# Kernel tuning notes

Hardware: AMD Instinct MI355X
Metric: run time of the kernel (lower is better)

## Reference

```python
import jax, jax.numpy as jnp
import numpy as np

B, IN, H = 16384, 128, 512
NH = 4
HD = H // NH


def setup_inputs() -> dict:
    key = jax.random.key(0)
    ks = jax.random.split(key, 20)
    s = lambda k, shape: jax.random.normal(k, shape, dtype=jnp.float32) * 0.05
    return {
        "x": jax.random.normal(ks[0], (B, IN), dtype=jnp.float32),
        "hidden_left": jax.random.normal(ks[1], (B, H), dtype=jnp.float32),
        "hidden_up": jax.random.normal(ks[2], (B, H), dtype=jnp.float32),
        "hidden_prev": jax.random.normal(ks[3], (B, H), dtype=jnp.float32),
        # input_proj
        "W_in": s(ks[4], (H, IN)),
        "b_in": jnp.zeros((H,), jnp.float32),
        # MultiheadAttention (packed qkv in-proj + out-proj), torch convention W:[out,in]
        "attn_in_w": s(ks[5], (3 * H, H)),
        "attn_in_b": jnp.zeros((3 * H,), jnp.float32),
        "attn_out_w": s(ks[6], (H, H)),
        "attn_out_b": jnp.zeros((H,), jnp.float32),
        # spatial_gate: Linear(3H -> H) then sigmoid
        "W_gate": s(ks[7], (H, 3 * H)),
        "b_gate": jnp.zeros((H,), jnp.float32),
        # GRUCell (torch layout: [3H, .] with r,z,n blocks)
        "gru_w_ih": s(ks[8], (3 * H, IN)),
        "gru_w_hh": s(ks[9], (3 * H, H)),
        "gru_b_ih": jnp.zeros((3 * H,), jnp.float32),
        "gru_b_hh": jnp.zeros((3 * H,), jnp.float32),
    }


def reference(x, hidden_left, hidden_up, hidden_prev,
              W_in, b_in, attn_in_w, attn_in_b, attn_out_w, attn_out_b,
              W_gate, b_gate, gru_w_ih, gru_w_hh, gru_b_ih, gru_b_hh):
    # input projection
    x_proj = x @ W_in.T + b_in  # [B, H]

    # spatial attention over the 2 neighbor states
    sp = jnp.stack([hidden_left, hidden_up], axis=1)          # [B, 2, H]
    qkv = sp @ attn_in_w.T + attn_in_b                        # [B, 2, 3H]
    q, k, v = jnp.split(qkv, 3, axis=-1)
    q = q.reshape(-1, 2, NH, HD)
    k = k.reshape(-1, 2, NH, HD)
    v = v.reshape(-1, 2, NH, HD)
    scores = jnp.einsum("bqhd,bkhd->bhqk", q, k) / jnp.sqrt(jnp.float32(HD))
    attn = jax.nn.softmax(scores, axis=-1)                    # [B, NH, 2, 2]
    ctx = jnp.einsum("bhqk,bkhd->bqhd", attn, v).reshape(-1, 2, H)
    sp_out = ctx @ attn_out_w.T + attn_out_b                  # [B, 2, H]
    spatial_combined = sp_out.mean(axis=1)                    # [B, H]

    # gated blend into previous hidden
    gate_in = jnp.concatenate([hidden_prev, spatial_combined, x_proj], axis=1)
    gate = jax.nn.sigmoid(gate_in @ W_gate.T + b_gate)
    enhanced_prev = hidden_prev + gate * spatial_combined

    # GRUCell(x, enhanced_prev), torch gate order r, z, n
    gi = x @ gru_w_ih.T + gru_b_ih                            # [B, 3H]
    gh = enhanced_prev @ gru_w_hh.T + gru_b_hh                # [B, 3H]
    i_r, i_z, i_n = jnp.split(gi, 3, axis=1)
    h_r, h_z, h_n = jnp.split(gh, 3, axis=1)
    r = jax.nn.sigmoid(i_r + h_r)
    z = jax.nn.sigmoid(i_z + h_z)
    n = jnp.tanh(i_n + r * h_n)
    new_hidden = (1.0 - z) * n + z * enhanced_prev
    # dropout is identity in eval mode
    return new_hidden
```

## Files before the change

### kernel.cpp

```cpp
#include <hip/hip_runtime.h>
#include <hip/hip_bf16.h>
#include <stdint.h>


#define NB 16384
#define NHEADS 4

typedef __attribute__((ext_vector_type(8))) __bf16 bf16x8;
typedef __attribute__((ext_vector_type(4))) float f32x4;
typedef __attribute__((ext_vector_type(8))) unsigned short u16x8;

__device__ __forceinline__ unsigned short f2bf(float f) {
  union { float f; unsigned int u; } v; v.f = f;
  unsigned int u = v.u;
  unsigned int r = (u + 0x7fffu + ((u >> 16) & 1u)) >> 16;
  return (unsigned short)r;
}
__device__ __forceinline__ float bf2f(unsigned short h) {
  union { unsigned int u; float f; } v; v.u = ((unsigned int)h) << 16;
  return v.f;
}
__device__ __forceinline__ float sigmoidf_(float x) {
  return 1.0f / (1.0f + __expf(-x));
}

#define J0 (512 * 128 / 8)
#define J1 (1536 * 128 / 8)
#define J2 (1536 * 512 / 8)
#define J3 (512 * 512 / 8)
#define J4 (512 * 1536 / 8)
#define J5 (1536 * 512 / 8)
#define J6 (NB * 128 / 8)
#define J7 (NB * 512 / 8)
#define J8 (NB * 512 / 8)
#define C1 (J0)
#define C2 (C1 + J1)
#define C3 (C2 + J2)
#define C4 (C3 + J3)
#define C5 (C4 + J4)
#define C6 (C5 + J5)
#define C7 (C6 + J6)
#define C8 (C7 + J7)
#define CT (C8 + J8)

struct CvtJobs {
  const float* src[9];
  unsigned short* dst[9];
};

__global__ void cvt_multi(CvtJobs j) {
  int g = blockIdx.x * blockDim.x + threadIdx.x;
  if (g >= CT) return;
  int k, base;
  if (g < C4) {
    if (g < C2) {
      if (g < C1) { k = 0; base = 0; } else { k = 1; base = C1; }
    } else {
      if (g < C3) { k = 2; base = C2; } else { k = 3; base = C3; }
    }
  } else {
    if (g < C6) {
      if (g < C5) { k = 4; base = C4; } else { k = 5; base = C5; }
    } else {
      if (g < C7) { k = 6; base = C6; }
      else if (g < C8) { k = 7; base = C7; }
      else { k = 8; base = C8; }
    }
  }
  int local = g - base;
  const float4* s = (const float4*)j.src[k] + (size_t)local * 2;
  float4 a = s[0], b = s[1];
  u16x8 o;
  o[0] = f2bf(a.x); o[1] = f2bf(a.y); o[2] = f2bf(a.z); o[3] = f2bf(a.w);
  o[4] = f2bf(b.x); o[5] = f2bf(b.y); o[6] = f2bf(b.z); o[7] = f2bf(b.w);
  *((u16x8*)j.dst[k] + local) = o;
}

__global__ void pack_hp(const float* __restrict__ hp,
                        unsigned short* __restrict__ gate_in) {
  int t = blockIdx.x * blockDim.x + threadIdx.x;
  int b = t >> 6;
  int j = (t & 63) * 8;
  const float4* s = (const float4*)(hp + (size_t)b * 512 + j);
  float4 a = s[0], c = s[1];
  u16x8 o;
  o[0] = f2bf(a.x); o[1] = f2bf(a.y); o[2] = f2bf(a.z); o[3] = f2bf(a.w);
  o[4] = f2bf(c.x); o[5] = f2bf(c.y); o[6] = f2bf(c.z); o[7] = f2bf(c.w);
  *(u16x8*)(gate_in + (size_t)b * 1536 + j) = o;
}

__device__ __forceinline__ void gl_lds16(const unsigned short* g, unsigned short* l) {
  __builtin_amdgcn_global_load_lds(
      (const __attribute__((address_space(1))) void*)g,
      (__attribute__((address_space(3))) void*)l, 16, 0, 0);
}

template <int EPI>
__global__ __launch_bounds__(512, 1) void gemm_big(
    const unsigned short* __restrict__ A, int lda,
    const unsigned short* __restrict__ W, int ldw,
    const float* __restrict__ bias, const float* __restrict__ bias2,
    int K, int ntx,
    unsigned short* __restrict__ outb, int ldob,
    unsigned short* __restrict__ outb2, int ldob2) {
  __shared__ unsigned short lds[65536];
  unsigned short* Asb = lds;
  unsigned short* Bsb = lds + 32768;
  const int tid = threadIdx.x;
  const int lane = tid & 63;
  const int wave = tid >> 6;

  const int nwg = gridDim.x;
  const int cpx = nwg >> 3;
  const int bid = blockIdx.x;
  const int id = (bid & 7) * cpx + (bid >> 3);
  const int bx = id % ntx;
  const int by = id / ntx;

  const int m0 = by * 256;
  const int n0 = bx * 256;
  const int ar0 = (wave >> 2) * 64;
  const int br0 = (wave & 3) * 32;

  f32x4 acc[4][4][2] = {};

  const int srow = tid >> 3;
  const int presw = (tid & 7) ^ (srow & 7);
  const unsigned short* Ag = A + (size_t)(m0 + srow) * lda + presw * 8;
  const unsigned short* Wg = W + (size_t)(n0 + srow) * ldw + presw * 8;
  unsigned short* Asd = Asb + tid * 8;
  unsigned short* Wsd = Bsb + tid * 8;

  auto stageA = [&](int buf, int h, int k0) {
    const unsigned short* s = Ag + (size_t)(h * 128) * lda + k0;
    unsigned short* d = Asd + buf * 16384 + h * 8192;
    gl_lds16(s, d);
    gl_lds16(s + (size_t)64 * lda, d + 4096);
  };
  auto stageB = [&](int buf, int h, int k0) {
    const unsigned short* s = Wg + (size_t)(h * 128) * ldw + k0;
    unsigned short* d = Wsd + buf * 16384 + h * 8192;
    gl_lds16(s, d);
    gl_lds16(s + (size_t)64 * ldw, d + 4096);
  };

  const int lrow = lane & 15;
  const int kq = (lane >> 4) * 8;
  const int sw = (lrow & 7) << 3;
  const int NT = K >> 6;

  stageA(0, 0, 0);
  stageB(0, 0, 0);
  stageB(0, 1, 0);
  stageA(0, 1, 0);
  asm volatile("s_waitcnt vmcnt(4)" ::: "memory");
  __builtin_amdgcn_s_barrier();

  bf16x8 a[4][2], b0[2][2], b1[2][2];

#define RD_A(X, H)                                                            \
  _Pragma("unroll") for (int m = 0; m < 4; ++m)                               \
  _Pragma("unroll") for (int kk = 0; kk < 2; ++kk)                            \
      a[m][kk] = *(const bf16x8*)&Asb[(X) * 16384 +                           \
                                      ((H) * 128 + ar0 + m * 16 + lrow) * 64 +\
                                      ((kk * 32 + kq) ^ sw)];
#define RD_B(X, H, DST)                                                       \
  _Pragma("unroll") for (int n = 0; n < 2; ++n)                               \
  _Pragma("unroll") for (int kk = 0; kk < 2; ++kk)                            \
      DST[n][kk] = *(const bf16x8*)&Bsb[(X) * 16384 +                         \
                                        ((H) * 128 + br0 + n * 16 + lrow) * 64 + \
                                        ((kk * 32 + kq) ^ sw)];
#define MFMA_Q(Q, BF)                                                         \
  __builtin_amdgcn_s_setprio(1);                                              \
  _Pragma("unroll") for (int m = 0; m < 4; ++m)                               \
  _Pragma("unroll") for (int n = 0; n < 2; ++n)                               \
  _Pragma("unroll") for (int kk = 0; kk < 2; ++kk)                            \
      acc[Q][m][n] = __builtin_amdgcn_mfma_f32_16x16x32_bf16(                 \
          a[m][kk], BF[n][kk], acc[Q][m][n], 0, 0, 0);                        \
  __builtin_amdgcn_s_setprio(0);
#define LGKM0                                                                 \
  asm volatile("s_waitcnt lgkmcnt(0)" ::: "memory");                          \
  __builtin_amdgcn_sched_barrier(0);
#define BAR __builtin_amdgcn_s_barrier();

  for (int t = 0; t < NT - 1; ++t) {
    const int X = t & 1, Y = X ^ 1;
    const int kn = (t + 1) << 6;
    RD_A(X, 0)
    RD_B(X, 0, b0)
    stageA(Y, 0, kn);
    stageB(Y, 0, kn);
    asm volatile("s_waitcnt vmcnt(4)" ::: "memory");
    BAR LGKM0
    MFMA_Q(0, b0)
    BAR
    RD_B(X, 1, b1)
    stageB(Y, 1, kn);
    BAR LGKM0
    MFMA_Q(1, b1)
    BAR
    RD_A(X, 1)
    stageA(Y, 1, kn);
    BAR LGKM0
    MFMA_Q(2, b1)
    BAR
    asm volatile("s_waitcnt vmcnt(4)" ::: "memory");
    BAR
    __builtin_amdgcn_sched_barrier(0);
    MFMA_Q(3, b0)
    BAR
  }
  {
    const int X = (NT - 1) & 1;
    RD_A(X, 0)
    RD_B(X, 0, b0)
    asm volatile("s_waitcnt vmcnt(0)" ::: "memory");
    BAR LGKM0
    MFMA_Q(0, b0)
    RD_B(X, 1, b1)
    LGKM0
    MFMA_Q(1, b1)
    RD_A(X, 1)
    LGKM0
    MFMA_Q(2, b1)
    MFMA_Q(3, b0)
  }
#undef RD_A
#undef RD_B
#undef MFMA_Q
#undef LGKM0
#undef BAR

  __syncthreads();
  unsigned short* ob = outb;
  int ld = ldob, ncof = n0;
  const float* bp = bias;
  if constexpr (EPI == 2) {
    if (n0 >= 512) { ob = outb2; ld = ldob2; ncof = n0 - 512; bp = bias2; }
  }
  const int qr[4] = {0, 0, 128, 128};
  const int qc[4] = {0, 128, 128, 0};
  const int ri = (lane >> 4) << 2;
#pragma unroll
  for (int q = 0; q < 4; ++q) {
#pragma unroll
    for (int n = 0; n < 2; ++n) {
      const int col = qc[q] + br0 + n * 16 + lrow;
      const float bv = bp ? bp[ncof + col] : 0.0f;
      const int g8 = col >> 3, c7 = col & 7;
#pragma unroll
      for (int m = 0; m < 4; ++m)
#pragma unroll
        for (int i = 0; i < 4; ++i) {
          const int row = qr[q] + ar0 + m * 16 + ri + i;
          lds[row * 256 + ((g8 ^ (row & 7)) << 3) + c7] =
              f2bf(acc[q][m][n][i] + bv);
        }
    }
  }
  __syncthreads();
#pragma unroll
  for (int jj = 0; jj < 16; ++jj) {
    int c = jj * 512 + tid;
    int row = c >> 5;
    int slot = c & 31;
    u16x8 v = *(const u16x8*)&lds[row * 256 + ((slot ^ (row & 7)) << 3)];
    *(u16x8*)&ob[(size_t)(m0 + row) * ld + ncof + slot * 8] = v;
  }
}

__global__ __launch_bounds__(512, 1) void g7_gru(
    const unsigned short* __restrict__ A, int lda,
    const unsigned short* __restrict__ W, int ldw,
    const float* __restrict__ b_hh, int K, int ntx,
    const unsigned short* __restrict__ gi,
    const unsigned short* __restrict__ enh,
    float* __restrict__ out) {
  __shared__ unsigned short lds[65536];
  unsigned short* Asb = lds;
  unsigned short* Bsb = lds + 16384;
  const int tid = threadIdx.x;
  const int lane = tid & 63;
  const int wave = tid >> 6;

  const int nwg = gridDim.x;
  const int cpx = nwg >> 3;
  const int bid = blockIdx.x;
  const int id = (bid & 7) * cpx + (bid >> 3);
  const int bx = id % ntx;
  const int by = id / ntx;

  const int m0 = by * 128;
  const int j0 = bx * 128;
  const int wm = (wave >> 2) * 64;
  const int wj = (wave & 3) * 32;

  f32x4 acc[4][6] = {};

  const int srow = tid >> 3;
  const int presw = (tid & 7) ^ (srow & 7);
  const unsigned short* Ag = A + (size_t)(m0 + srow) * lda + presw * 8;
  unsigned short* Asd = Asb + tid * 8;
  unsigned short* Bsd = Bsb + tid * 8;

  auto stage = [&](int buf, int k0) {
    gl_lds16(Ag + k0, Asd + buf * 8192);
    gl_lds16(Ag + (size_t)64 * lda + k0, Asd + buf * 8192 + 4096);
#pragma unroll
    for (int l = 0; l < 6; ++l) {
      const int gate = l >> 1;
      const int rr = (l & 1) * 64 + srow;
      gl_lds16(W + (size_t)(gate * 512 + j0 + rr) * ldw + presw * 8 + k0,
               Bsd + buf * 24576 + l * 4096);
    }
  };

  stage(0, 0);
  int cur = 0;
  const int lrow = lane & 15;
  const int kq = (lane >> 4) * 8;
  const int sw = (lrow & 7) << 3;

  for (int k0 = 0; k0 < K; k0 += 64) {
    if (k0 + 64 < K) {
      stage(cur ^ 1, k0 + 64);
      asm volatile("s_waitcnt vmcnt(8)" ::: "memory");
    } else {
      asm volatile("s_waitcnt vmcnt(0)" ::: "memory");
    }
    __builtin_amdgcn_s_barrier();
    const unsigned short* Ab = Asb + cur * 8192;
    const unsigned short* Bb = Bsb + cur * 24576;
    bf16x8 a[4][2], b[6][2];
#pragma unroll
    for (int m = 0; m < 4; ++m)
#pragma unroll
      for (int kk = 0; kk < 2; ++kk)
        a[m][kk] = *(const bf16x8*)&Ab[(wm + m * 16 + lrow) * 64 +
                                       ((kk * 32 + kq) ^ sw)];
#pragma unroll
    for (int f = 0; f < 6; ++f)
#pragma unroll
      for (int kk = 0; kk < 2; ++kk) {
        const int brow = (f >> 1) * 128 + wj + (f & 1) * 16 + lrow;
        b[f][kk] = *(const bf16x8*)&Bb[brow * 64 + ((kk * 32 + kq) ^ sw)];
      }
    __builtin_amdgcn_s_setprio(1);
#pragma unroll
    for (int m = 0; m < 4; ++m)
#pragma unroll
      for (int f = 0; f < 6; ++f)
#pragma unroll
        for (int kk = 0; kk < 2; ++kk)
          acc[m][f] = __builtin_amdgcn_mfma_f32_16x16x32_bf16(a[m][kk], b[f][kk],
                                                              acc[m][f], 0, 0, 0);
    __builtin_amdgcn_s_setprio(0);
    __builtin_amdgcn_s_barrier();
    cur ^= 1;
  }

  const int r0 = m0 + wm + ((lane >> 4) << 2);
#pragma unroll
  for (int jj = 0; jj < 2; ++jj) {
    const int j = j0 + wj + jj * 16 + lrow;
    const float bhr = b_hh[j];
    const float bhz = b_hh[512 + j];
    const float bhn = b_hh[1024 + j];
#pragma unroll
    for (int m = 0; m < 4; ++m) {
#pragma unroll
      for (int i = 0; i < 4; ++i) {
        const int row = r0 + m * 16 + i;
        const size_t gb = (size_t)row * 1536 + j;
        float ir = bf2f(gi[gb]);
        float iz = bf2f(gi[gb + 512]);
        float in_ = bf2f(gi[gb + 1024]);
        float hr = acc[m][jj][i] + bhr;
        float hz = acc[m][2 + jj][i] + bhz;
        float hn = acc[m][4 + jj][i] + bhn;
        float rr = sigmoidf_(ir + hr);
        float zz = sigmoidf_(iz + hz);
        float nn = tanhf(in_ + rr * hn);
        float ev = bf2f(enh[(size_t)row * 512 + j]);
        out[(size_t)row * 512 + j] = (1.0f - zz) * nn + zz * ev;
      }
    }
  }
}

template <int EPI>
__global__ __launch_bounds__(256, 2) void gemm_bt(
    const unsigned short* __restrict__ A, int lda,
    const unsigned short* __restrict__ W, int ldw,
    const float* __restrict__ bias, int K, int ntx,
    unsigned short* __restrict__ outb, int ldob,
    const unsigned short* __restrict__ gin) {
  __shared__ unsigned short As[2][128 * 64];
  __shared__ unsigned short Ws[2][128 * 64];
  const int tid = threadIdx.x;
  const int lane = tid & 63;
  const int wave = tid >> 6;

  const int nwg = gridDim.x;
  const int cpx = nwg >> 3;
  const int bid = blockIdx.x;
  const int id = (bid & 7) * cpx + (bid >> 3);
  const int bx = id % ntx;
  const int by = id / ntx;

  const int m0 = by * 128;
  const int n0 = bx * 128;
  const int wm = (wave >> 1) * 64;
  const int wn = (wave & 1) * 64;

  f32x4 acc[4][4] = {};

  const int srow = tid >> 3;
  const int sslot = (tid & 7) ^ (srow & 7);
  const unsigned short* Ag = A + (size_t)(m0 + srow) * lda + sslot * 8;
  const unsigned short* Wg = W + (size_t)(n0 + srow) * ldw + sslot * 8;
  unsigned short* Asd = &As[0][tid * 8];
  unsigned short* Wsd = &Ws[0][tid * 8];

  auto stage = [&](int buf, int k0) {
#pragma unroll
    for (int i = 0; i < 4; ++i) {
      gl_lds16(Ag + (size_t)(i * 32) * lda + k0, Asd + buf * 8192 + i * 2048);
      gl_lds16(Wg + (size_t)(i * 32) * ldw + k0, Wsd + buf * 8192 + i * 2048);
    }
  };

  stage(0, 0);
  int cur = 0;
  const int lrow = lane & 15;
  const int kq = (lane >> 4) * 8;
  const int sw = (lrow & 7) << 3;

  for (int k0 = 0; k0 < K; k0 += 64) {
    if (k0 + 64 < K) {
      stage(cur ^ 1, k0 + 64);
      asm volatile("s_waitcnt vmcnt(8)" ::: "memory");
    } else {
      asm volatile("s_waitcnt vmcnt(0)" ::: "memory");
    }
    __builtin_amdgcn_s_barrier();
#pragma unroll
    for (int kk = 0; kk < 2; ++kk) {
      const int kr = kk * 32 + kq;
      const int ki = kr ^ sw;
      bf16x8 af[4], wf[4];
#pragma unroll
      for (int m = 0; m < 4; ++m)
        af[m] = *(const bf16x8*)&As[cur][(wm + m * 16 + lrow) * 64 + ki];
#pragma unroll
      for (int n = 0; n < 4; ++n)
        wf[n] = *(const bf16x8*)&Ws[cur][(wn + n * 16 + lrow) * 64 + ki];
#pragma unroll
      for (int m = 0; m < 4; ++m)
#pragma unroll
        for (int n = 0; n < 4; ++n)
          acc[m][n] = __builtin_amdgcn_mfma_f32_16x16x32_bf16(af[m], wf[n],
                                                              acc[m][n], 0, 0, 0);
    }
    __builtin_amdgcn_s_barrier();
    cur ^= 1;
  }

  if constexpr (EPI == 1) {
    const int r0 = m0 + wm + ((lane >> 4) << 2);
    const int c0 = n0 + wn + lrow;
#pragma unroll
    for (int n = 0; n < 4; ++n) {
      const int col = c0 + n * 16;
      const float bv = bias ? bias[col] : 0.0f;
#pragma unroll
      for (int m = 0; m < 4; ++m) {
#pragma unroll
        for (int i = 0; i < 4; ++i) {
          const int row = r0 + m * 16 + i;
          float g = sigmoidf_(acc[m][n][i] + bv);
          float hpv = bf2f(gin[(size_t)row * 1536 + col]);
          float sc = bf2f(gin[(size_t)row * 1536 + 512 + col]);
          float e = hpv + g * sc;
          outb[(size_t)row * 512 + col] = f2bf(e);
        }
      }
    }
  } else {
    unsigned short* Cs = &As[0][0];
    const int r0l = wm + ((lane >> 4) << 2);
    const int c0l = wn + lrow;
#pragma unroll
    for (int n = 0; n < 4; ++n) {
      const int col = c0l + n * 16;
      const float bv = bias ? bias[n0 + col] : 0.0f;
#pragma unroll
      for (int m = 0; m < 4; ++m)
#pragma unroll
        for (int i = 0; i < 4; ++i)
          Cs[(r0l + m * 16 + i) * 128 + col] = f2bf(acc[m][n][i] + bv);
    }
    __syncthreads();
#pragma unroll
    for (int jj = 0; jj < 8; ++jj) {
      int c = jj * 256 + tid;
      int row = c >> 4;
      int slot = c & 15;
      u16x8 v = *(const u16x8*)&Cs[row * 128 + slot * 8];
      *(u16x8*)&outb[(size_t)(m0 + row) * ldob + n0 + slot * 8] = v;
    }
  }
}

__global__ void attn_fuse(const unsigned short* __restrict__ qkvl,
                          const unsigned short* __restrict__ qkvu,
                          unsigned short* __restrict__ ctx) {
  int t = blockIdx.x * blockDim.x + threadIdx.x;
  int g = t >> 4;
  int l = t & 15;
  int b = g >> 2, h = g & 3;
  const size_t base = (size_t)b * 1536 + h * 128 + l * 8;
  u16x8 q0 = *(const u16x8*)(qkvl + base);
  u16x8 k0 = *(const u16x8*)(qkvl + base + 512);
  u16x8 v0 = *(const u16x8*)(qkvl + base + 1024);
  u16x8 q1 = *(const u16x8*)(qkvu + base);
  u16x8 k1 = *(const u16x8*)(qkvu + base + 512);
  u16x8 v1 = *(const u16x8*)(qkvu + base + 1024);
  float s00 = 0.f, s01 = 0.f, s10 = 0.f, s11 = 0.f;
  float v0f[8], v1f[8];
#pragma unroll
  for (int i = 0; i < 8; ++i) {
    float q0f = bf2f(q0[i]), q1f = bf2f(q1[i]);
    float k0f = bf2f(k0[i]), k1f = bf2f(k1[i]);
    v0f[i] = bf2f(v0[i]); v1f[i] = bf2f(v1[i]);
    s00 += q0f * k0f; s01 += q0f * k1f;
    s10 += q1f * k0f; s11 += q1f * k1f;
  }
#pragma unroll
  for (int off = 1; off < 16; off <<= 1) {
    s00 += __shfl_xor(s00, off);
    s01 += __shfl_xor(s01, off);
    s10 += __shfl_xor(s10, off);
    s11 += __shfl_xor(s11, off);
  }
  const float scale = 0.0883883476483184f;
  s00 *= scale; s01 *= scale; s10 *= scale; s11 *= scale;
  float m0 = fmaxf(s00, s01), m1 = fmaxf(s10, s11);
  float a00 = __expf(s00 - m0), a01 = __expf(s01 - m0);
  float a10 = __expf(s10 - m1), a11 = __expf(s11 - m1);
  float c0 = 0.5f * (a00 / (a00 + a01) + a10 / (a10 + a11));
  float c1 = 0.5f * (a01 / (a00 + a01) + a11 / (a10 + a11));
  u16x8 o;
#pragma unroll
  for (int i = 0; i < 8; ++i) o[i] = f2bf(c0 * v0f[i] + c1 * v1f[i]);
  *(u16x8*)(ctx + (size_t)b * 512 + h * 128 + l * 8) = o;
}

extern "C" void kernel_launch(void* const* d_in, const int* in_sizes, int n_in,
                              void* d_out, int out_size, void* d_ws, size_t ws_size,
                              hipStream_t stream) {
  const float* x = (const float*)d_in[0];
  const float* hl = (const float*)d_in[1];
  const float* hu = (const float*)d_in[2];
  const float* hp = (const float*)d_in[3];
  const float* W_in = (const float*)d_in[4];
  const float* b_in = (const float*)d_in[5];
  const float* attn_in_w = (const float*)d_in[6];
  const float* attn_in_b = (const float*)d_in[7];
  const float* attn_out_w = (const float*)d_in[8];
  const float* attn_out_b = (const float*)d_in[9];
  const float* W_gate = (const float*)d_in[10];
  const float* b_gate = (const float*)d_in[11];
  const float* gru_w_ih = (const float*)d_in[12];
  const float* gru_w_hh = (const float*)d_in[13];
  const float* gru_b_ih = (const float*)d_in[14];
  const float* gru_b_hh = (const float*)d_in[15];

  char* ws = (char*)d_ws;
  size_t off = 0;
  auto alloc = [&](size_t bytes) {
    void* p = ws + off;
    off += (bytes + 255) & ~(size_t)255;
    return p;
  };
  unsigned short* wComb = (unsigned short*)alloc((size_t)2048 * 128 * 2);
  unsigned short* wAin  = (unsigned short*)alloc((size_t)1536 * 512 * 2);
  unsigned short* wAout = (unsigned short*)alloc((size_t)512 * 512 * 2);
  unsigned short* wGate = (unsigned short*)alloc((size_t)512 * 1536 * 2);
  unsigned short* wHh   = (unsigned short*)alloc((size_t)1536 * 512 * 2);
  unsigned short* xb   = (unsigned short*)alloc((size_t)NB * 128 * 2);
  unsigned short* hlub = (unsigned short*)alloc((size_t)2 * NB * 512 * 2);
  unsigned short* gate_in = (unsigned short*)alloc((size_t)NB * 1536 * 2);
  unsigned short* qkvb = (unsigned short*)alloc((size_t)2 * NB * 1536 * 2);
  unsigned short* ctxb = (unsigned short*)alloc((size_t)NB * 512 * 2);
  unsigned short* enhb = (unsigned short*)alloc((size_t)NB * 512 * 2);
  unsigned short* qkvl = qkvb;
  unsigned short* qkvu = qkvb + (size_t)NB * 1536;
  unsigned short* gi = qkvl;

  (void)ws_size; (void)in_sizes; (void)n_in; (void)out_size;

  const int T = 256;

  CvtJobs jobs;
  jobs.src[0] = W_in;       jobs.dst[0] = wComb;
  jobs.src[1] = gru_w_ih;   jobs.dst[1] = wComb + (size_t)512 * 128;
  jobs.src[2] = attn_in_w;  jobs.dst[2] = wAin;
  jobs.src[3] = attn_out_w; jobs.dst[3] = wAout;
  jobs.src[4] = W_gate;     jobs.dst[4] = wGate;
  jobs.src[5] = gru_w_hh;   jobs.dst[5] = wHh;
  jobs.src[6] = x;          jobs.dst[6] = xb;
  jobs.src[7] = hl;         jobs.dst[7] = hlub;
  jobs.src[8] = hu;         jobs.dst[8] = hlub + (size_t)NB * 512;
  cvt_multi<<<(CT + T - 1) / T, T, 0, stream>>>(jobs);
  pack_hp<<<NB * 64 / T, T, 0, stream>>>(hp, gate_in);

  const int MTB = NB / 256;
  const int MTS = NB / 128;

  gemm_big<0><<<6 * 2 * MTB, dim3(512), 0, stream>>>(hlub, 512, wAin, 512,
                                                     attn_in_b, nullptr, 512, 6,
                                                     qkvb, 1536, nullptr, 0);
  attn_fuse<<<NB * NHEADS * 16 / T, T, 0, stream>>>(qkvl, qkvu, ctxb);
  gemm_bt<0><<<4 * MTS, T, 0, stream>>>(ctxb, 512, wAout, 512, attn_out_b,
                                        512, 4,
                                        gate_in + 512, 1536, nullptr);
  gemm_big<2><<<8 * MTB, dim3(512), 0, stream>>>(xb, 128, wComb, 128,
                                                 b_in, gru_b_ih, 128, 8,
                                                 gate_in + 1024, 1536, gi, 1536);
  gemm_bt<1><<<4 * MTS, T, 0, stream>>>(gate_in, 1536, wGate, 1536, b_gate,
                                        1536, 4,
                                        enhb, 512, gate_in);
  g7_gru<<<4 * MTS, dim3(512), 0, stream>>>(enhb, 512, wHh, 512, gru_b_hh,
                                            512, 4, gi, enhb, (float*)d_out);
}
```

Baseline: 271.1 us.

## Fuse QKV projection with 2-token attention and interleave neighbor rows

Hidden_left and hidden_up rows are interleaved during bf16 conversion so each 128-row tile holds both neighbors of 64 batch elements. A new kernel computes the per-head Q/K/V projection tile and the attention softmax/mix in LDS, writing only the context. This removes the round trip of the full QKV intermediate through global memory and one launch. The hidden_prev pack is folded into the conversion kernel. The cost is a smaller per-block N tile (384 columns) with more LDS traffic and epilogue work inside the GEMM.

```diff
diff --git a/kernel.cpp b/kernel.cpp
--- a/kernel.cpp
+++ b/kernel.cpp
@@ -4,7 +4,6 @@
 
 
 #define NB 16384
-#define NHEADS 4
 
 typedef __attribute__((ext_vector_type(8))) __bf16 bf16x8;
 typedef __attribute__((ext_vector_type(4))) float f32x4;
@@ -33,6 +32,7 @@
 #define J6 (NB * 128 / 8)
 #define J7 (NB * 512 / 8)
 #define J8 (NB * 512 / 8)
+#define J9 (NB * 512 / 8)
 #define C1 (J0)
 #define C2 (C1 + J1)
 #define C3 (C2 + J2)
@@ -41,11 +41,12 @@
 #define C6 (C5 + J5)
 #define C7 (C6 + J6)
 #define C8 (C7 + J7)
-#define CT (C8 + J8)
+#define C9 (C8 + J8)
+#define CT (C9 + J9)
 
 struct CvtJobs {
-  const float* src[9];
-  unsigned short* dst[9];
+  const float* src[10];
+  unsigned short* dst[10];
 };
 
 __global__ void cvt_multi(CvtJobs j) {
@@ -64,7 +65,8 @@
     } else {
       if (g < C7) { k = 6; base = C6; }
       else if (g < C8) { k = 7; base = C7; }
-      else { k = 8; base = C8; }
+      else if (g < C9) { k = 8; base = C8; }
+      else { k = 9; base = C9; }
     }
   }
   int local = g - base;
@@ -73,20 +75,12 @@
   u16x8 o;
   o[0] = f2bf(a.x); o[1] = f2bf(a.y); o[2] = f2bf(a.z); o[3] = f2bf(a.w);
   o[4] = f2bf(b.x); o[5] = f2bf(b.y); o[6] = f2bf(b.z); o[7] = f2bf(b.w);
-  *((u16x8*)j.dst[k] + local) = o;
-}
-
-__global__ void pack_hp(const float* __restrict__ hp,
-                        unsigned short* __restrict__ gate_in) {
-  int t = blockIdx.x * blockDim.x + threadIdx.x;
-  int b = t >> 6;
-  int j = (t & 63) * 8;
-  const float4* s = (const float4*)(hp + (size_t)b * 512 + j);
-  float4 a = s[0], c = s[1];
-  u16x8 o;
-  o[0] = f2bf(a.x); o[1] = f2bf(a.y); o[2] = f2bf(a.z); o[3] = f2bf(a.w);
-  o[4] = f2bf(c.x); o[5] = f2bf(c.y); o[6] = f2bf(c.z); o[7] = f2bf(c.w);
-  *(u16x8*)(gate_in + (size_t)b * 1536 + j) = o;
+  size_t didx;
+  if (k == 7)      didx = ((size_t)(local >> 6) << 7) + (local & 63);
+  else if (k == 8) didx = ((size_t)(local >> 6) << 7) + 64 + (local & 63);
+  else if (k == 9) didx = (size_t)(local >> 6) * 192 + (local & 63);
+  else             didx = (size_t)local;
+  *((u16x8*)j.dst[k] + didx) = o;
 }
 
 __device__ __forceinline__ void gl_lds16(const unsigned short* g, unsigned short* l) {
@@ -269,6 +263,155 @@
   }
 }
 
+__global__ __launch_bounds__(512, 1) void qkva(
+    const unsigned short* __restrict__ A,
+    const unsigned short* __restrict__ W,
+    const float* __restrict__ bias,
+    unsigned short* __restrict__ ctx) {
+  __shared__ unsigned short lds[65536];
+  unsigned short* Asb = lds;
+  unsigned short* Bsb = lds + 16384;
+  const int tid = threadIdx.x;
+  const int lane = tid & 63;
+  const int wave = tid >> 6;
+
+  const int nwg = gridDim.x;
+  const int cpx = nwg >> 3;
+  const int bid = blockIdx.x;
+  const int id = (bid & 7) * cpx + (bid >> 3);
+  const int bx = id & 3;
+  const int by = id >> 2;
+
+  const int m0 = by * 128;
+  const int h0 = bx * 128;
+  const int wm = (wave >> 2) * 64;
+  const int wj = (wave & 3) * 32;
+
+  f32x4 acc[4][6] = {};
+
+  const int srow = tid >> 3;
+  const int presw = (tid & 7) ^ (srow & 7);
+  const unsigned short* Ag = A + (size_t)(m0 + srow) * 512 + presw * 8;
+  unsigned short* Asd = Asb + tid * 8;
+  unsigned short* Bsd = Bsb + tid * 8;
+
+  auto stage = [&](int buf, int k0) {
+    gl_lds16(Ag + k0, Asd + buf * 8192);
+    gl_lds16(Ag + (size_t)64 * 512 + k0, Asd + buf * 8192 + 4096);
+#pragma unroll
+    for (int l = 0; l < 6; ++l) {
+      const int gate = l >> 1;
+      const int rr = (l & 1) * 64 + srow;
+      gl_lds16(W + (size_t)(gate * 512 + h0 + rr) * 512 + presw * 8 + k0,
+               Bsd + buf * 24576 + l * 4096);
+    }
+  };
+
+  stage(0, 0);
+  int cur = 0;
+  const int lrow = lane & 15;
+  const int kq = (lane >> 4) * 8;
+  const int sw = (lrow & 7) << 3;
+
+  for (int k0 = 0; k0 < 512; k0 += 64) {
+    if (k0 + 64 < 512) {
+      stage(cur ^ 1, k0 + 64);
+      asm volatile("s_waitcnt vmcnt(8)" ::: "memory");
+    } else {
+      asm volatile("s_waitcnt vmcnt(0)" ::: "memory");
+    }
+    __builtin_amdgcn_s_barrier();
+    const unsigned short* Ab = Asb + cur * 8192;
+    const unsigned short* Bb = Bsb + cur * 24576;
+    bf16x8 a[4][2], b[6][2];
+#pragma unroll
+    for (int m = 0; m < 4; ++m)
+#pragma unroll
+      for (int kk = 0; kk < 2; ++kk)
+        a[m][kk] = *(const bf16x8*)&Ab[(wm + m * 16 + lrow) * 64 +
+                                       ((kk * 32 + kq) ^ sw)];
+#pragma unroll
+    for (int f = 0; f < 6; ++f)
+#pragma unroll
+      for (int kk = 0; kk < 2; ++kk) {
+        const int brow = (f >> 1) * 128 + wj + (f & 1) * 16 + lrow;
+        b[f][kk] = *(const bf16x8*)&Bb[brow * 64 + ((kk * 32 + kq) ^ sw)];
+      }
+    __builtin_amdgcn_s_setprio(1);
+#pragma unroll
+    for (int m = 0; m < 4; ++m)
+#pragma unroll
+      for (int f = 0; f < 6; ++f)
+#pragma unroll
+        for (int kk = 0; kk < 2; ++kk)
+          acc[m][f] = __builtin_amdgcn_mfma_f32_16x16x32_bf16(a[m][kk], b[f][kk],
+                                                              acc[m][f], 0, 0, 0);
+    __builtin_amdgcn_s_setprio(0);
+    __builtin_amdgcn_s_barrier();
+    cur ^= 1;
+  }
+
+  __syncthreads();
+  const int ri = (lane >> 4) << 2;
+#pragma unroll
+  for (int f = 0; f < 6; ++f) {
+    const int gate = f >> 1;
+    const int col = wj + (f & 1) * 16 + lrow;
+    const float bv = bias[gate * 512 + h0 + col];
+#pragma unroll
+    for (int m = 0; m < 4; ++m)
+#pragma unroll
+      for (int i = 0; i < 4; ++i) {
+        const int row = wm + m * 16 + ri + i;
+        lds[gate * 17408 + row * 136 + col] = f2bf(acc[m][f][i] + bv);
+      }
+  }
+  __syncthreads();
+
+  const int l = tid & 15;
+  const int grp = tid >> 4;
+#pragma unroll
+  for (int it = 0; it < 2; ++it) {
+    const int p = it * 32 + grp;
+    const int r0 = 2 * p, r1 = 2 * p + 1;
+    u16x8 q0 = *(const u16x8*)&lds[r0 * 136 + l * 8];
+    u16x8 q1 = *(const u16x8*)&lds[r1 * 136 + l * 8];
+    u16x8 k0 = *(const u16x8*)&lds[17408 + r0 * 136 + l * 8];
+    u16x8 k1 = *(const u16x8*)&lds[17408 + r1 * 136 + l * 8];
+    u16x8 v0 = *(const u16x8*)&lds[34816 + r0 * 136 + l * 8];
+    u16x8 v1 = *(const u16x8*)&lds[34816 + r1 * 136 + l * 8];
+    float s00 = 0.f, s01 = 0.f, s10 = 0.f, s11 = 0.f;
+    float v0f[8], v1f[8];
+#pragma unroll
+    for (int i = 0; i < 8; ++i) {
+      float q0f = bf2f(q0[i]), q1f = bf2f(q1[i]);
+      float k0f = bf2f(k0[i]), k1f = bf2f(k1[i]);
+      v0f[i] = bf2f(v0[i]); v1f[i] = bf2f(v1[i]);
+      s00 += q0f * k0f; s01 += q0f * k1f;
+      s10 += q1f * k0f; s11 += q1f * k1f;
+    }
+#pragma unroll
+    for (int off = 1; off < 16; off <<= 1) {
+      s00 += __shfl_xor(s00, off);
+      s01 += __shfl_xor(s01, off);
+      s10 += __shfl_xor(s10, off);
+      s11 += __shfl_xor(s11, off);
+    }
+    const float scale = 0.0883883476483184f;
+    s00 *= scale; s01 *= scale; s10 *= scale; s11 *= scale;
+    float mx0 = fmaxf(s00, s01), mx1 = fmaxf(s10, s11);
+    float a00 = __expf(s00 - mx0), a01 = __expf(s01 - mx0);
+    float a10 = __expf(s10 - mx1), a11 = __expf(s11 - mx1);
+    float c0 = 0.5f * (a00 / (a00 + a01) + a10 / (a10 + a11));
+    float c1 = 0.5f * (a01 / (a00 + a01) + a11 / (a10 + a11));
+    u16x8 o;
+#pragma unroll
+    for (int i = 0; i < 8; ++i) o[i] = f2bf(c0 * v0f[i] + c1 * v1f[i]);
+    const int bglob = (m0 >> 1) + p;
+    *(u16x8*)&ctx[(size_t)bglob * 512 + h0 + l * 8] = o;
+  }
+}
+
 __global__ __launch_bounds__(512, 1) void g7_gru(
     const unsigned short* __restrict__ A, int lda,
     const unsigned short* __restrict__ W, int ldw,
@@ -510,50 +653,6 @@
       *(u16x8*)&outb[(size_t)(m0 + row) * ldob + n0 + slot * 8] = v;
     }
   }
-}
-
-__global__ void attn_fuse(const unsigned short* __restrict__ qkvl,
-                          const unsigned short* __restrict__ qkvu,
-                          unsigned short* __restrict__ ctx) {
-  int t = blockIdx.x * blockDim.x + threadIdx.x;
-  int g = t >> 4;
-  int l = t & 15;
-  int b = g >> 2, h = g & 3;
-  const size_t base = (size_t)b * 1536 + h * 128 + l * 8;
-  u16x8 q0 = *(const u16x8*)(qkvl + base);
-  u16x8 k0 = *(const u16x8*)(qkvl + base + 512);
-  u16x8 v0 = *(const u16x8*)(qkvl + base + 1024);
-  u16x8 q1 = *(const u16x8*)(qkvu + base);
-  u16x8 k1 = *(const u16x8*)(qkvu + base + 512);
-  u16x8 v1 = *(const u16x8*)(qkvu + base + 1024);
-  float s00 = 0.f, s01 = 0.f, s10 = 0.f, s11 = 0.f;
-  float v0f[8], v1f[8];
-#pragma unroll
-  for (int i = 0; i < 8; ++i) {
-    float q0f = bf2f(q0[i]), q1f = bf2f(q1[i]);
-    float k0f = bf2f(k0[i]), k1f = bf2f(k1[i]);
-    v0f[i] = bf2f(v0[i]); v1f[i] = bf2f(v1[i]);
-    s00 += q0f * k0f; s01 += q0f * k1f;
-    s10 += q1f * k0f; s11 += q1f * k1f;
-  }
-#pragma unroll
-  for (int off = 1; off < 16; off <<= 1) {
-    s00 += __shfl_xor(s00, off);
-    s01 += __shfl_xor(s01, off);
-    s10 += __shfl_xor(s10, off);
-    s11 += __shfl_xor(s11, off);
-  }
-  const float scale = 0.0883883476483184f;
-  s00 *= scale; s01 *= scale; s10 *= scale; s11 *= scale;
-  float m0 = fmaxf(s00, s01), m1 = fmaxf(s10, s11);
-  float a00 = __expf(s00 - m0), a01 = __expf(s01 - m0);
-  float a10 = __expf(s10 - m1), a11 = __expf(s11 - m1);
-  float c0 = 0.5f * (a00 / (a00 + a01) + a10 / (a10 + a11));
-  float c1 = 0.5f * (a01 / (a00 + a01) + a11 / (a10 + a11));
-  u16x8 o;
-#pragma unroll
-  for (int i = 0; i < 8; ++i) o[i] = f2bf(c0 * v0f[i] + c1 * v1f[i]);
-  *(u16x8*)(ctx + (size_t)b * 512 + h * 128 + l * 8) = o;
 }
 
 extern "C" void kernel_launch(void* const* d_in, const int* in_sizes, int n_in,
@@ -589,14 +688,12 @@
   unsigned short* wGate = (unsigned short*)alloc((size_t)512 * 1536 * 2);
   unsigned short* wHh   = (unsigned short*)alloc((size_t)1536 * 512 * 2);
   unsigned short* xb   = (unsigned short*)alloc((size_t)NB * 128 * 2);
-  unsigned short* hlub = (unsigned short*)alloc((size_t)2 * NB * 512 * 2);
+  unsigned short* hlib = (unsigned short*)alloc((size_t)2 * NB * 512 * 2);
   unsigned short* gate_in = (unsigned short*)alloc((size_t)NB * 1536 * 2);
   unsigned short* qkvb = (unsigned short*)alloc((size_t)2 * NB * 1536 * 2);
   unsigned short* ctxb = (unsigned short*)alloc((size_t)NB * 512 * 2);
   unsigned short* enhb = (unsigned short*)alloc((size_t)NB * 512 * 2);
-  unsigned short* qkvl = qkvb;
-  unsigned short* qkvu = qkvb + (size_t)NB * 1536;
-  unsigned short* gi = qkvl;
+  unsigned short* gi = qkvb;
 
   (void)ws_size; (void)in_sizes; (void)n_in; (void)out_size;
 
@@ -610,18 +707,15 @@
   jobs.src[4] = W_gate;     jobs.dst[4] = wGate;
   jobs.src[5] = gru_w_hh;   jobs.dst[5] = wHh;
   jobs.src[6] = x;          jobs.dst[6] = xb;
-  jobs.src[7] = hl;         jobs.dst[7] = hlub;
-  jobs.src[8] = hu;         jobs.dst[8] = hlub + (size_t)NB * 512;
+  jobs.src[7] = hl;         jobs.dst[7] = hlib;
+  jobs.src[8] = hu;         jobs.dst[8] = hlib;
+  jobs.src[9] = hp;         jobs.dst[9] = gate_in;
   cvt_multi<<<(CT + T - 1) / T, T, 0, stream>>>(jobs);
-  pack_hp<<<NB * 64 / T, T, 0, stream>>>(hp, gate_in);
 
   const int MTB = NB / 256;
   const int MTS = NB / 128;
 
-  gemm_big<0><<<6 * 2 * MTB, dim3(512), 0, stream>>>(hlub, 512, wAin, 512,
-                                                     attn_in_b, nullptr, 512, 6,
-                                                     qkvb, 1536, nullptr, 0);
-  attn_fuse<<<NB * NHEADS * 16 / T, T, 0, stream>>>(qkvl, qkvu, ctxb);
+  qkva<<<1024, dim3(512), 0, stream>>>(hlib, wAin, attn_in_b, ctxb);
   gemm_bt<0><<<4 * MTS, T, 0, stream>>>(ctxb, 512, wAout, 512, attn_out_b,
                                         512, 4,
                                         gate_in + 512, 1536, nullptr);
```

After: 236.3 us. 1.15x faster.
